# Optimization experiments

Hardware: AMD Instinct MI355X
Metric: run time of the kernel (lower is better)

The kernel has to match this reference:

```python
import jax, jax.numpy as jnp
import numpy as np

N = 100000
E = 1600000
D_IN, D_HID, D_OUT = 128, 128, 128


def gcn_conv(x, edge_index, W, b):
    """PyG GCNConv with default symmetric normalization and added self-loops.
    out = D^{-1/2} (A + I) D^{-1/2} (x W) + b, edge weights = 1.
    """
    n = x.shape[0]
    h = x @ W                                   # [N, D_out]
    src, dst = edge_index[0], edge_index[1]     # messages flow src -> dst
    ones = jnp.ones(src.shape[0], dtype=x.dtype)
    # degree includes the self-loop (+1), computed on the target index as in PyG
    deg = jax.ops.segment_sum(ones, dst, num_segments=n) + 1.0  # [N]
    dinv = jax.lax.rsqrt(deg)                   # deg >= 1 so safe
    norm = dinv[src] * dinv[dst]                # [E]
    msg = h[src] * norm[:, None]                # [E, D_out]
    agg = jax.ops.segment_sum(msg, dst, num_segments=n)
    # self-loop contribution: norm = dinv_i * dinv_i = 1/deg_i
    out = agg + h * (dinv * dinv)[:, None] + b
    return out


def layer_norm(x, gamma, beta, eps=1e-5):
    mu = jnp.mean(x, axis=-1, keepdims=True)
    var = jnp.mean(jnp.square(x - mu), axis=-1, keepdims=True)
    return (x - mu) * jax.lax.rsqrt(var + eps) * gamma + beta


def setup_inputs() -> dict:
    key = jax.random.key(0)
    ks = jax.random.split(key, 8)
    x = jax.random.normal(ks[0], (N, D_IN), dtype=jnp.float32)
    edge_index = jax.random.randint(ks[1], (2, E), 0, N, dtype=jnp.int64)
    s1 = 1.0 / np.sqrt(D_IN)
    s2 = 1.0 / np.sqrt(D_HID)
    W1 = jax.random.uniform(ks[2], (D_IN, D_HID), jnp.float32, -s1, s1)
    b1 = jnp.zeros((D_HID,), jnp.float32)
    W2 = jax.random.uniform(ks[3], (D_HID, D_OUT), jnp.float32, -s2, s2)
    b2 = jnp.zeros((D_OUT,), jnp.float32)
    gamma = jnp.ones((D_OUT,), jnp.float32)
    beta = jnp.zeros((D_OUT,), jnp.float32)
    return {"x": x, "edge_index": edge_index, "W1": W1, "b1": b1,
            "W2": W2, "b2": b2, "gamma": gamma, "beta": beta}


def reference(x, edge_index, W1, b1, W2, b2, gamma, beta):
    h = gcn_conv(x, edge_index, W1, b1)
    h = jax.nn.relu(h)
    # dropout is identity in eval mode (deterministic reference)
    h = gcn_conv(h, edge_index, W2, b2)
    return layer_norm(h, gamma, beta)
```

## Files before the change

kernel.cpp:

```cpp
#include <hip/hip_runtime.h>


#define N_NODES 100000
#define N_EDGES 1600000
#define NBLK_N  391
#define NB      391
#define BKT_CAP 4736
#define BIN_GRID 391
#define GEMM_GRID 1563
#define MM_GRID 1563

typedef unsigned int  u32;
typedef unsigned short u16;
typedef unsigned char u8;
typedef unsigned long long u64;
typedef __attribute__((ext_vector_type(8))) short bf16x8;
typedef __attribute__((ext_vector_type(4))) float f32x4;

__device__ __forceinline__ float bflo(u32 u){ return __uint_as_float(u << 16); }
__device__ __forceinline__ float bfhi(u32 u){ return __uint_as_float(u & 0xFFFF0000u); }
__device__ __forceinline__ u32 f2b(float f){
  u32 u = __float_as_uint(f);
  return (u + 0x7FFFu + ((u >> 16) & 1u)) >> 16;
}
__device__ __forceinline__ u32 pack2(float a, float b){ return f2b(a) | (f2b(b) << 16); }
__device__ __forceinline__ u32 clampN(int s){
  u32 u = (u32)s;
  return (u < (u32)N_NODES) ? u : (u32)(N_NODES - 1);
}

__global__ __launch_bounds__(64) void detect(const int* __restrict__ ei,
                                             int* __restrict__ flags){
  int l = threadIdx.x;
  int nzodd = (ei[2 * l + 1] != 0) ? 1 : 0;
  #pragma unroll
  for (int o = 32; o > 0; o >>= 1) nzodd += __shfl_xor(nzodd, o, 64);
  if (l == 0) flags[1] = (nzodd == 0) ? 1 : 0;
}


__device__ __forceinline__ void prep_body(const float* __restrict__ W,
                                          u16* __restrict__ dst, int tid){
  #pragma unroll
  for (int i = 0; i < 8; ++i){
    int fid   = tid + i * 256;
    int lane  = fid & 63;
    int kb    = (fid >> 6) & 3;
    int ntile = fid >> 8;
    int n  = ntile * 16 + (lane & 15);
    int k0 = kb * 32 + (lane >> 4) * 8;
    u16 tmp[8];
    #pragma unroll
    for (int j = 0; j < 8; ++j) tmp[j] = (u16)f2b(W[(k0 + j) * 128 + n]);
    *(bf16x8*)(dst + (size_t)fid * 8) = *(const bf16x8*)tmp;
  }
}

__global__ __launch_bounds__(256) void prep_frags(const float* __restrict__ W1,
                                                  const float* __restrict__ W2,
                                                  u16* __restrict__ w1f,
                                                  u16* __restrict__ w2f){
  prep_body(blockIdx.x ? W2 : W1, blockIdx.x ? w2f : w1f, threadIdx.x);
}


__device__ __forceinline__ void gemm_tail(const u16* __restrict__ wfrag,
                                          const bf16x8 afrag[4],
                                          int rowbase, int lane,
                                          u16* __restrict__ Hout, int nrows){
  const int m = lane & 15, q = lane >> 4;
  f32x4 acc[8];
  #pragma unroll
  for (int n = 0; n < 8; ++n) acc[n] = (f32x4){0.f, 0.f, 0.f, 0.f};
  #pragma unroll
  for (int n = 0; n < 8; ++n){
    #pragma unroll
    for (int kb = 0; kb < 4; ++kb){
      bf16x8 bfrag = *(const bf16x8*)(wfrag + ((size_t)(n * 4 + kb) * 64 + lane) * 8);
      acc[n] = __builtin_amdgcn_mfma_f32_16x16x32_bf16(afrag[kb], bfrag, acc[n], 0, 0, 0);
    }
  }
  #pragma unroll
  for (int r = 0; r < 4; ++r){
    int orow = rowbase + q * 4 + r;
    if (orow < nrows){
      u16* Or = Hout + (size_t)orow * 128 + m;
      #pragma unroll
      for (int n = 0; n < 8; ++n) Or[n * 16] = (u16)f2b(acc[n][r]);
    }
  }
}

__device__ __forceinline__ void gemm_f32_body(const u16* __restrict__ wfragG,
                                              const float* __restrict__ A,
                                              u16* __restrict__ Hout, int nrows, int bid){
  const int lane = threadIdx.x & 63;
  const int wv   = threadIdx.x >> 6;
  const int rowbase = bid * 64 + wv * 16;
  const int row  = rowbase + (lane & 15);
  const int rowc = (row < nrows) ? row : (nrows - 1);
  const int q    = lane >> 4;
  bf16x8 afrag[4];
  const float* Ar = A + (size_t)rowc * 128;
  #pragma unroll
  for (int kb = 0; kb < 4; ++kb){
    f32x4 p0 = *(const f32x4*)(Ar + kb * 32 + q * 8);
    f32x4 p1 = *(const f32x4*)(Ar + kb * 32 + q * 8 + 4);
    bf16x8 f;
    f[0] = (short)f2b(p0[0]); f[1] = (short)f2b(p0[1]);
    f[2] = (short)f2b(p0[2]); f[3] = (short)f2b(p0[3]);
    f[4] = (short)f2b(p1[0]); f[5] = (short)f2b(p1[1]);
    f[6] = (short)f2b(p1[2]); f[7] = (short)f2b(p1[3]);
    afrag[kb] = f;
  }
  gemm_tail(wfragG, afrag, rowbase, lane, Hout, nrows);
}


__device__ __forceinline__ void binA_body(u32* smem ,
                                          const int* __restrict__ ei,
                                          u32* __restrict__ binned,
                                          u32* __restrict__ bucket_fill, int bb){
  u32* cnt   = smem;
  u32* gbase = smem + NB;
  u32* flagp = smem + 2 * NB;
  const int tid = threadIdx.x;
  for (int i = tid; i < NB; i += 256) cnt[i] = 0;
  if (tid < 64){
    int nz = (ei[2 * tid + 1] != 0) ? 1 : 0;
    u64 b = __ballot(nz);
    if (tid == 0) *flagp = (b == 0ull) ? 1u : 0u;
  }
  __syncthreads();
  const int i64  = (int)*flagp;
  const int base = bb * 4096;
  u32 pk[16], rk[16], bk[16];
  #pragma unroll
  for (int j = 0; j < 16; ++j){
    int e = base + tid + j * 256;
    bk[j] = 0xFFFFFFFFu;
    if (e < N_EDGES){
      int dsti = i64 ? ei[2 * N_EDGES + 2 * e] : ei[N_EDGES + e];
      int srci = i64 ? ei[2 * e]               : ei[e];
      u32 ud = clampN(dsti), us = clampN(srci);
      u32 b = ud >> 8;
      bk[j] = b;
      pk[j] = us | ((ud & 255u) << 17);
      rk[j] = atomicAdd(&cnt[b], 1u);
    }
  }
  __syncthreads();
  for (int i = tid; i < NB; i += 256){
    u32 c = cnt[i];
    gbase[i] = c ? atomicAdd(&bucket_fill[i], c) : 0u;
  }
  __syncthreads();
  #pragma unroll
  for (int j = 0; j < 16; ++j){
    if (bk[j] != 0xFFFFFFFFu){
      u32 idx = gbase[bk[j]] + rk[j];
      if (idx < BKT_CAP) binned[(size_t)bk[j] * BKT_CAP + idx] = pk[j];
    }
  }
}


__global__ __launch_bounds__(256) void bin_prep(const int* __restrict__ ei,
                                                u32* __restrict__ binned,
                                                u32* __restrict__ bucket_fill,
                                                const float* __restrict__ W1,
                                                const float* __restrict__ W2,
                                                u16* __restrict__ w1f,
                                                u16* __restrict__ w2f){
  __shared__ u32 smem[2 * NB + 1];
  if (blockIdx.x < BIN_GRID){
    binA_body(smem, ei, binned, bucket_fill, blockIdx.x);
  } else {
    int pb = blockIdx.x - BIN_GRID;
    prep_body(pb ? W2 : W1, pb ? w2f : w1f, threadIdx.x);
  }
}


__device__ __forceinline__ void fill_sort_body(u32* smem ,
                                               const u32* __restrict__ binned,
                                               const u32* __restrict__ bucket_fill,
                                               int* __restrict__ offs,
                                               float* __restrict__ dinv,
                                               int* __restrict__ srclist, int b){
  u32* cnt = smem;
  u32* sc  = smem + 256;
  u32* red = smem + 512;
  const int tid = threadIdx.x;
  cnt[tid] = 0;

  u32 v = 0;
  for (int i = tid; i < b; i += 256){
    u32 f = bucket_fill[i];
    v += (f > BKT_CAP) ? BKT_CAP : f;
  }
  red[tid] = v;
  __syncthreads();
  for (int o = 128; o > 0; o >>= 1){
    if (tid < o) red[tid] += red[tid + o];
    __syncthreads();
  }
  const u32 base = red[0];

  u32 n = bucket_fill[b]; if (n > BKT_CAP) n = BKT_CAP;
  const u32* eb = binned + (size_t)b * BKT_CAP;

  for (u32 i = tid; i < n; i += 256)
    atomicAdd(&cnt[eb[i] >> 17], 1u);
  __syncthreads();

  u32 own = cnt[tid];
  sc[tid] = own;
  __syncthreads();
  for (int o = 1; o < 256; o <<= 1){
    u32 add = (tid >= o) ? sc[tid - o] : 0;
    __syncthreads();
    sc[tid] += add;
    __syncthreads();
  }
  u32 pex = sc[tid] - own;

  const u32 node = ((u32)b << 8) + tid;
  if (node < (u32)N_NODES){
    offs[node] = (int)(base + pex);
    dinv[node] = rsqrtf((float)own + 1.0f);
  }
  if (b == NB - 1 && tid == 0) offs[N_NODES] = (int)(base + n);

  __syncthreads();
  sc[tid]  = pex;
  cnt[tid] = 0;
  __syncthreads();

  for (u32 i = tid; i < n; i += 256){
    u32 pk = eb[i];
    u32 d  = pk >> 17;
    u32 r  = atomicAdd(&cnt[d], 1u);
    srclist[base + sc[d] + r] = (int)(pk & 0x1FFFFu);
  }
}


__global__ __launch_bounds__(256) void fused_fs_gemm(const u32* __restrict__ binned,
                                                     const u32* __restrict__ bucket_fill,
                                                     int* __restrict__ offs,
                                                     float* __restrict__ dinv,
                                                     int* __restrict__ srclist,
                                                     const float* __restrict__ A,
                                                     const u16* __restrict__ w1frag,
                                                     u16* __restrict__ Hout){
  __shared__ u32 smem[768];
  if (blockIdx.x < NB){
    fill_sort_body(smem, binned, bucket_fill, offs, dinv, srclist, blockIdx.x);
  } else {
    gemm_f32_body(w1frag, A, Hout, N_NODES, blockIdx.x - NB);
  }
}

__global__ __launch_bounds__(256) void gemm_f32in(const float* __restrict__ A,
                                                  const u16* __restrict__ wfragG,
                                                  u16* __restrict__ Hout){
  gemm_f32_body(wfragG, A, Hout, N_NODES, blockIdx.x);
}


__global__ __launch_bounds__(256) void count_deg(const int* __restrict__ ei,
                                                 const int* __restrict__ flags,
                                                 int* __restrict__ deg){
  int e   = blockIdx.x * 256 + threadIdx.x;
  int i64 = flags[1];
  int dst = i64 ? ei[2 * N_EDGES + 2 * e] : ei[N_EDGES + e];
  if ((unsigned)dst < (unsigned)N_NODES) atomicAdd(&deg[dst], 1);
}

__global__ __launch_bounds__(256) void fill_edges(const int* __restrict__ ei,
                                                  const int* __restrict__ flags,
                                                  int* __restrict__ woff,
                                                  int* __restrict__ srclist){
  int e   = blockIdx.x * 256 + threadIdx.x;
  int i64 = flags[1];
  int dst = i64 ? ei[2 * N_EDGES + 2 * e] : ei[N_EDGES + e];
  int src = i64 ? ei[2 * e]               : ei[e];
  if ((unsigned)dst < (unsigned)N_NODES){
    int p = atomicAdd(&woff[dst], 1);
    if ((unsigned)p < (unsigned)N_EDGES) srclist[p] = clampN(src);
  }
}

__global__ __launch_bounds__(256) void scan1(const int* __restrict__ deg,
                                             int* __restrict__ offs,
                                             int* __restrict__ bsum,
                                             float* __restrict__ dinv){
  __shared__ int sh[256];
  int t = threadIdx.x;
  int i = blockIdx.x * 256 + t;
  int v = (i < N_NODES) ? deg[i] : 0;
  if (i < N_NODES) dinv[i] = rsqrtf((float)v + 1.0f);
  sh[t] = v;
  __syncthreads();
  for (int o = 1; o < 256; o <<= 1){
    int add = (t >= o) ? sh[t - o] : 0;
    __syncthreads();
    sh[t] += add;
    __syncthreads();
  }
  if (i < N_NODES) offs[i] = sh[t] - v;
  if (t == 255)    bsum[blockIdx.x] = sh[255];
}

__global__ __launch_bounds__(512) void scan2(const int* __restrict__ bsum,
                                             int* __restrict__ bofs){
  __shared__ int sh[512];
  int t = threadIdx.x;
  int v = (t < NBLK_N) ? bsum[t] : 0;
  sh[t] = v;
  __syncthreads();
  for (int o = 1; o < 512; o <<= 1){
    int add = (t >= o) ? sh[t - o] : 0;
    __syncthreads();
    sh[t] += add;
    __syncthreads();
  }
  if (t < NBLK_N) bofs[t] = sh[t] - v;
}

__global__ __launch_bounds__(256) void finalize_offs(int* __restrict__ offs,
                                                     const int* __restrict__ bofs,
                                                     int* __restrict__ woff){
  int i = blockIdx.x * 256 + threadIdx.x;
  if (i < N_NODES){
    int o = offs[i] + bofs[blockIdx.x];
    offs[i] = o;
    woff[i] = o;
  }
  if (i == 0) offs[N_NODES] = N_EDGES;
}


#define GATHER_EDGE(sv, A0, A1)                         \
  { u32 s_ = (u32)(sv);                                 \
    float w_ = dinv[s_];                                \
    u32 h_ = H[s_ * 64 + lane];                         \
    A0 = fmaf(w_, bflo(h_), A0);                        \
    A1 = fmaf(w_, bfhi(h_), A1); }

#define GATHER_BODY                                     \
  int beg = offs[node], end = offs[node + 1];           \
  if (end > N_EDGES) end = N_EDGES;                     \
  if (beg < 0 || beg > end) beg = end;                  \
  float a0 = 0.f, a1 = 0.f, c0 = 0.f, c1 = 0.f;         \
  int e = beg;                                          \
  for (; e + 8 <= end; e += 8){                         \
    int s0=srcl[e],s1=srcl[e+1],s2=srcl[e+2],s3=srcl[e+3]; \
    int s4=srcl[e+4],s5=srcl[e+5],s6=srcl[e+6],s7=srcl[e+7]; \
    GATHER_EDGE(s0,a0,a1) GATHER_EDGE(s1,c0,c1)         \
    GATHER_EDGE(s2,a0,a1) GATHER_EDGE(s3,c0,c1)         \
    GATHER_EDGE(s4,a0,a1) GATHER_EDGE(s5,c0,c1)         \
    GATHER_EDGE(s6,a0,a1) GATHER_EDGE(s7,c0,c1)         \
  }                                                     \
  for (; e + 4 <= end; e += 4){                         \
    int s0=srcl[e],s1=srcl[e+1],s2=srcl[e+2],s3=srcl[e+3]; \
    GATHER_EDGE(s0,a0,a1) GATHER_EDGE(s1,c0,c1)         \
    GATHER_EDGE(s2,a0,a1) GATHER_EDGE(s3,c0,c1)         \
  }                                                     \
  for (; e < end; ++e){ int s0=srcl[e]; GATHER_EDGE(s0,a0,a1) } \
  a0 += c0;  a1 += c1;                                  \
  float di = dinv[node];                                \
  u32 hs = H[(u32)node * 64 + lane];                    \
  float v0 = fmaf(a0, di, fmaf(bflo(hs), di * di, bb0)); \
  float v1 = fmaf(a1, di, fmaf(bfhi(hs), di * di, bb1));


__global__ __launch_bounds__(256) void gather_relu_mm(const int* __restrict__ offs,
                                                      const int* __restrict__ srcl,
                                                      const u32* __restrict__ H,
                                                      const float* __restrict__ dinv,
                                                      const float* __restrict__ bias,
                                                      const u16* __restrict__ w2frag,
                                                      u16* __restrict__ H2){
  __shared__ u32 xs[64 * 68];
  const int lane = threadIdx.x & 63;
  const int wv   = threadIdx.x >> 6;
  const int m = lane & 15, q = lane >> 4;
  const int nodebase = blockIdx.x * 64 + wv * 16;
  u32* xw = xs + wv * (16 * 68);
  const float bb0 = bias[2 * lane], bb1 = bias[2 * lane + 1];

  #pragma unroll 1
  for (int j = 0; j < 16; ++j){
    int node = nodebase + j;
    if (node >= N_NODES) node = N_NODES - 1;
    GATHER_BODY
    xw[j * 68 + lane] = pack2(fmaxf(v0, 0.f), fmaxf(v1, 0.f));
  }

  bf16x8 afrag[4];
  #pragma unroll
  for (int kb = 0; kb < 4; ++kb)
    afrag[kb] = *(const bf16x8*)(xw + m * 68 + kb * 16 + q * 4);

  #pragma unroll
  for (int n = 0; n < 8; ++n){
    f32x4 acc = (f32x4){0.f, 0.f, 0.f, 0.f};
    #pragma unroll
    for (int kb = 0; kb < 4; ++kb){
      bf16x8 bfrag = *(const bf16x8*)(w2frag + ((size_t)(n * 4 + kb) * 64 + lane) * 8);
      acc = __builtin_amdgcn_mfma_f32_16x16x32_bf16(afrag[kb], bfrag, acc, 0, 0, 0);
    }
    const int col = n * 16 + m;
    #pragma unroll
    for (int r = 0; r < 4; ++r){
      const int row = nodebase + q * 4 + r;
      if (row < N_NODES) H2[(size_t)row * 128 + col] = (u16)f2b(acc[r]);
    }
  }
}


__global__ __launch_bounds__(256) void gather_ln(const int* __restrict__ offs,
                                                 const int* __restrict__ srcl,
                                                 const u32* __restrict__ H,
                                                 const float* __restrict__ dinv,
                                                 const float* __restrict__ bias,
                                                 const float* __restrict__ gamma,
                                                 const float* __restrict__ beta,
                                                 float* __restrict__ out){
  const int node = blockIdx.x * 4 + (threadIdx.x >> 6);
  const int lane = threadIdx.x & 63;
  const float bb0 = bias[2 * lane], bb1 = bias[2 * lane + 1];
  GATHER_BODY

  float s2 = v0 + v1;
  #pragma unroll
  for (int o = 32; o > 0; o >>= 1) s2 += __shfl_xor(s2, o, 64);
  float mu = s2 * 0.0078125f;
  float d0 = v0 - mu, d1 = v1 - mu;
  float qq = d0 * d0 + d1 * d1;
  #pragma unroll
  for (int o = 32; o > 0; o >>= 1) qq += __shfl_xor(qq, o, 64);
  float rr = rsqrtf(qq * 0.0078125f + 1e-5f);

  float g0 = gamma[2 * lane], g1 = gamma[2 * lane + 1];
  float t0 = beta[2 * lane],  t1 = beta[2 * lane + 1];
  *(float2*)(out + (size_t)node * 128 + 2 * lane) =
      make_float2(fmaf(d0 * rr, g0, t0), fmaf(d1 * rr, g1, t1));
}


extern "C" void kernel_launch(void* const* d_in, const int* in_sizes, int n_in,
                              void* d_out, int out_size, void* d_ws, size_t ws_size,
                              hipStream_t stream){
  const float* x  = (const float*)d_in[0];
  const int*   ei = (const int*)d_in[1];
  const float* W1 = (const float*)d_in[2];
  const float* b1 = (const float*)d_in[3];
  const float* W2 = (const float*)d_in[4];
  const float* b2 = (const float*)d_in[5];
  const float* gm = (const float*)d_in[6];
  const float* bt = (const float*)d_in[7];

  char* ws = (char*)d_ws;
  size_t off = 0;
  auto carve = [&](size_t bytes) -> void* {
    void* p = ws + off;
    off = (off + bytes + 255) & ~(size_t)255;
    return p;
  };
  int*   flags       = (int*)  carve(64);
  u16*   w1frag      = (u16*)  carve(128 * 128 * 2);
  u16*   w2frag      = (u16*)  carve(128 * 128 * 2);
  u32*   bucket_fill = (u32*)  carve(NB * 4);
  int*   offs        = (int*)  carve((size_t)(N_NODES + 1) * 4);
  float* dinv        = (float*)carve((size_t)N_NODES * 4);
  int*   srclist     = (int*)  carve((size_t)N_EDGES * 4);
  int*   deg         = (int*)  carve((size_t)N_NODES * 4);
  int*   bsum        = (int*)  carve(2048);
  int*   bofs        = (int*)  carve(2048);

  size_t bin_bytes = (size_t)NB * BKT_CAP * 4;
  u32* binned = (u32*)carve(bin_bytes);
  bool use_binned = (ws_size >= off);
  if (!use_binned) off = (size_t)((char*)binned - ws);

  size_t h_bytes = (size_t)N_NODES * 128 * 2;
  u32* H1 = (u32*)d_out;
  u32* H2 = (ws_size >= off + h_bytes) ? (u32*)carve(h_bytes) : (u32*)d_in[0];

  if (use_binned){
    hipMemsetAsync(bucket_fill, 0, NB * 4, stream);
    bin_prep      <<<BIN_GRID + 2, 256, 0, stream>>>(ei, binned, bucket_fill,
                                                     W1, W2, w1frag, w2frag);
    fused_fs_gemm <<<NB + GEMM_GRID, 256, 0, stream>>>(binned, bucket_fill, offs, dinv,
                                                       srclist, x, w1frag, (u16*)H1);
  } else {
    prep_frags    <<<2,             256, 0, stream>>>(W1, W2, w1frag, w2frag);
    hipMemsetAsync(deg, 0, (size_t)N_NODES * 4, stream);
    detect        <<<1,             64,  0, stream>>>(ei, flags);
    count_deg     <<<N_EDGES / 256, 256, 0, stream>>>(ei, flags, deg);
    scan1         <<<NBLK_N,        256, 0, stream>>>(deg, offs, bsum, dinv);
    scan2         <<<1,             512, 0, stream>>>(bsum, bofs);
    finalize_offs <<<NBLK_N,        256, 0, stream>>>(offs, bofs, deg );
    fill_edges    <<<N_EDGES / 256, 256, 0, stream>>>(ei, flags, deg , srclist);
    gemm_f32in    <<<GEMM_GRID,     256, 0, stream>>>(x, w1frag, (u16*)H1);
  }

  gather_relu_mm <<<MM_GRID,     256, 0, stream>>>(offs, srclist, H1, dinv, b1,
                                                   w2frag, (u16*)H2);
  gather_ln      <<<N_NODES / 4, 256, 0, stream>>>(offs, srclist, H2, dinv, b2, gm, bt,
                                                   (float*)d_out);
}
```

Before: 300.8 us.

## Fuse memset, binning, GEMM and fill-sort into one cooperative kernel

Measured after the change: 628.3 us. 2.09x slower.

```diff
diff --git a/kernel.cpp b/kernel.cpp
--- a/kernel.cpp
+++ b/kernel.cpp
@@ -1,4 +1,7 @@
 #include <hip/hip_runtime.h>
+#include <hip/hip_cooperative_groups.h>
+
+namespace cg = cooperative_groups;
 
 
 #define N_NODES 100000
@@ -9,6 +12,8 @@
 #define BIN_GRID 391
 #define GEMM_GRID 1563
 #define MM_GRID 1563
+#define MEGA_GEMM 782
+#define MEGA_GRID (BIN_GRID + MEGA_GEMM)
 
 typedef unsigned int  u32;
 typedef unsigned short u16;
@@ -165,6 +170,108 @@
 }
 
 
+__device__ __forceinline__ void fill_sort_body(u32* smem ,
+                                               const u32* __restrict__ binned,
+                                               const u32* __restrict__ bucket_fill,
+                                               int* __restrict__ offs,
+                                               float* __restrict__ dinv,
+                                               int* __restrict__ srclist, int b){
+  u32* cnt = smem;
+  u32* sc  = smem + 256;
+  u32* red = smem + 512;
+  const int tid = threadIdx.x;
+  cnt[tid] = 0;
+
+  u32 v = 0;
+  for (int i = tid; i < b; i += 256){
+    u32 f = bucket_fill[i];
+    v += (f > BKT_CAP) ? BKT_CAP : f;
+  }
+  red[tid] = v;
+  __syncthreads();
+  for (int o = 128; o > 0; o >>= 1){
+    if (tid < o) red[tid] += red[tid + o];
+    __syncthreads();
+  }
+  const u32 base = red[0];
+
+  u32 n = bucket_fill[b]; if (n > BKT_CAP) n = BKT_CAP;
+  const u32* eb = binned + (size_t)b * BKT_CAP;
+
+  for (u32 i = tid; i < n; i += 256)
+    atomicAdd(&cnt[eb[i] >> 17], 1u);
+  __syncthreads();
+
+  u32 own = cnt[tid];
+  sc[tid] = own;
+  __syncthreads();
+  for (int o = 1; o < 256; o <<= 1){
+    u32 add = (tid >= o) ? sc[tid - o] : 0;
+    __syncthreads();
+    sc[tid] += add;
+    __syncthreads();
+  }
+  u32 pex = sc[tid] - own;
+
+  const u32 node = ((u32)b << 8) + tid;
+  if (node < (u32)N_NODES){
+    offs[node] = (int)(base + pex);
+    dinv[node] = rsqrtf((float)own + 1.0f);
+  }
+  if (b == NB - 1 && tid == 0) offs[N_NODES] = (int)(base + n);
+
+  __syncthreads();
+  sc[tid]  = pex;
+  cnt[tid] = 0;
+  __syncthreads();
+
+  for (u32 i = tid; i < n; i += 256){
+    u32 pk = eb[i];
+    u32 d  = pk >> 17;
+    u32 r  = atomicAdd(&cnt[d], 1u);
+    srclist[base + sc[d] + r] = (int)(pk & 0x1FFFFu);
+  }
+}
+
+
+__global__ __launch_bounds__(256, 5) void mega_prep(const int* __restrict__ ei,
+                                                    u32* __restrict__ binned,
+                                                    u32* __restrict__ bucket_fill,
+                                                    const float* __restrict__ W1,
+                                                    const float* __restrict__ W2,
+                                                    u16* __restrict__ w1f,
+                                                    u16* __restrict__ w2f,
+                                                    const float* __restrict__ x,
+                                                    u16* __restrict__ H1,
+                                                    int* __restrict__ offs,
+                                                    float* __restrict__ dinv,
+                                                    int* __restrict__ srclist){
+  __shared__ u32 smem[2 * NB + 1];
+  cg::grid_group grid = cg::this_grid();
+
+  if (blockIdx.x == 0){
+    for (int i = threadIdx.x; i < NB; i += 256) bucket_fill[i] = 0;
+  } else if (blockIdx.x == 1){
+    prep_body(W1, w1f, threadIdx.x);
+  } else if (blockIdx.x == 2){
+    prep_body(W2, w2f, threadIdx.x);
+  }
+  grid.sync();
+
+  if (blockIdx.x < BIN_GRID){
+    binA_body(smem, ei, binned, bucket_fill, blockIdx.x);
+  } else {
+    int t0 = 2 * (blockIdx.x - BIN_GRID);
+    if (t0 < GEMM_GRID)     gemm_f32_body(w1f, x, H1, N_NODES, t0);
+    if (t0 + 1 < GEMM_GRID) gemm_f32_body(w1f, x, H1, N_NODES, t0 + 1);
+  }
+  grid.sync();
+
+  if (blockIdx.x < NB)
+    fill_sort_body(smem, binned, bucket_fill, offs, dinv, srclist, blockIdx.x);
+}
+
+
 __global__ __launch_bounds__(256) void bin_prep(const int* __restrict__ ei,
                                                 u32* __restrict__ binned,
                                                 u32* __restrict__ bucket_fill,
@@ -180,71 +287,6 @@
     prep_body(pb ? W2 : W1, pb ? w2f : w1f, threadIdx.x);
   }
 }
-
-
-__device__ __forceinline__ void fill_sort_body(u32* smem ,
-                                               const u32* __restrict__ binned,
-                                               const u32* __restrict__ bucket_fill,
-                                               int* __restrict__ offs,
-                                               float* __restrict__ dinv,
-                                               int* __restrict__ srclist, int b){
-  u32* cnt = smem;
-  u32* sc  = smem + 256;
-  u32* red = smem + 512;
-  const int tid = threadIdx.x;
-  cnt[tid] = 0;
-
-  u32 v = 0;
-  for (int i = tid; i < b; i += 256){
-    u32 f = bucket_fill[i];
-    v += (f > BKT_CAP) ? BKT_CAP : f;
-  }
-  red[tid] = v;
-  __syncthreads();
-  for (int o = 128; o > 0; o >>= 1){
-    if (tid < o) red[tid] += red[tid + o];
-    __syncthreads();
-  }
-  const u32 base = red[0];
-
-  u32 n = bucket_fill[b]; if (n > BKT_CAP) n = BKT_CAP;
-  const u32* eb = binned + (size_t)b * BKT_CAP;
-
-  for (u32 i = tid; i < n; i += 256)
-    atomicAdd(&cnt[eb[i] >> 17], 1u);
-  __syncthreads();
-
-  u32 own = cnt[tid];
-  sc[tid] = own;
-  __syncthreads();
-  for (int o = 1; o < 256; o <<= 1){
-    u32 add = (tid >= o) ? sc[tid - o] : 0;
-    __syncthreads();
-    sc[tid] += add;
-    __syncthreads();
-  }
-  u32 pex = sc[tid] - own;
-
-  const u32 node = ((u32)b << 8) + tid;
-  if (node < (u32)N_NODES){
-    offs[node] = (int)(base + pex);
-    dinv[node] = rsqrtf((float)own + 1.0f);
-  }
-  if (b == NB - 1 && tid == 0) offs[N_NODES] = (int)(base + n);
-
-  __syncthreads();
-  sc[tid]  = pex;
-  cnt[tid] = 0;
-  __syncthreads();
-
-  for (u32 i = tid; i < n; i += 256){
-    u32 pk = eb[i];
-    u32 d  = pk >> 17;
-    u32 r  = atomicAdd(&cnt[d], 1u);
-    srclist[base + sc[d] + r] = (int)(pk & 0x1FFFFu);
-  }
-}
-
 
 __global__ __launch_bounds__(256) void fused_fs_gemm(const u32* __restrict__ binned,
                                                      const u32* __restrict__ bucket_fill,
@@ -492,11 +534,21 @@
   u32* H2 = (ws_size >= off + h_bytes) ? (u32*)carve(h_bytes) : (u32*)d_in[0];
 
   if (use_binned){
-    hipMemsetAsync(bucket_fill, 0, NB * 4, stream);
-    bin_prep      <<<BIN_GRID + 2, 256, 0, stream>>>(ei, binned, bucket_fill,
-                                                     W1, W2, w1frag, w2frag);
-    fused_fs_gemm <<<NB + GEMM_GRID, 256, 0, stream>>>(binned, bucket_fill, offs, dinv,
-                                                       srclist, x, w1frag, (u16*)H1);
+    u16* H1u = (u16*)H1;
+    void* args[] = {(void*)&ei, (void*)&binned, (void*)&bucket_fill, (void*)&W1,
+                    (void*)&W2, (void*)&w1frag, (void*)&w2frag, (void*)&x,
+                    (void*)&H1u, (void*)&offs, (void*)&dinv, (void*)&srclist};
+    hipError_t ce = hipLaunchCooperativeKernel((const void*)mega_prep,
+                                               dim3(MEGA_GRID), dim3(256),
+                                               args, 0, stream);
+    if (ce != hipSuccess){
+      hipMemsetAsync(bucket_fill, 0, NB * 4, stream);
+      bin_prep      <<<BIN_GRID + 2, 256, 0, stream>>>(ei, binned, bucket_fill,
+                                                       W1, W2, w1frag, w2frag);
+      fused_fs_gemm <<<NB + GEMM_GRID, 256, 0, stream>>>(binned, bucket_fill, offs,
+                                                         dinv, srclist, x, w1frag,
+                                                         (u16*)H1);
+    }
   } else {
     prep_frags    <<<2,             256, 0, stream>>>(W1, W2, w1frag, w2frag);
     hipMemsetAsync(deg, 0, (size_t)N_NODES * 4, stream);
```
